# Kernel optimization log

Hardware: AMD Instinct MI355X
Metric: run time of the kernel (lower is better)

Reference implementation:

```python
import jax, jax.numpy as jnp
import numpy as np

C = 512
NH = 8
HD = C // NH
GROUPS = 8
EPS = 1e-5

def group_norm(x, w, b):
    # x: [B,C,H,W], 8 groups
    B, Cc, H, W = x.shape
    xg = x.reshape(B, GROUPS, Cc // GROUPS, H, W)
    mu = xg.mean(axis=(2, 3, 4), keepdims=True)
    var = xg.var(axis=(2, 3, 4), keepdims=True)
    xn = (xg - mu) * jax.lax.rsqrt(var + EPS)
    xn = xn.reshape(B, Cc, H, W)
    return xn * w[None, :, None, None] + b[None, :, None, None]

def conv1x1(x, w, b):
    # w: [O,C], b: [O]
    return jnp.einsum('oc,bchw->bohw', w, x) + b[None, :, None, None]

def setup_inputs() -> dict:
    key = jax.random.key(0)
    ks = jax.random.split(key, 12)
    s = 1.0 / np.sqrt(C)
    inp = {
        'x': jax.random.normal(ks[0], (8, C, 32, 32), dtype=jnp.float32),
        'norm_w': jnp.ones((C,), jnp.float32),
        'norm_b': jnp.zeros((C,), jnp.float32),
        'qw': jax.random.uniform(ks[1], (C, C), jnp.float32, -s, s),
        'qb': jax.random.uniform(ks[2], (C,), jnp.float32, -s, s),
        'kw': jax.random.uniform(ks[3], (C, C), jnp.float32, -s, s),
        'kb': jax.random.uniform(ks[4], (C,), jnp.float32, -s, s),
        'vw': jax.random.uniform(ks[5], (C, C), jnp.float32, -s, s),
        'vb': jax.random.uniform(ks[6], (C,), jnp.float32, -s, s),
        'pw': jax.random.uniform(ks[7], (C, C), jnp.float32, -s, s),
        'pb': jax.random.uniform(ks[8], (C,), jnp.float32, -s, s),
    }
    return inp

def reference(x, norm_w, norm_b, qw, qb, kw, kb, vw, vb, pw, pb):
    b, c, h, w = x.shape
    scale = HD ** (-0.5)
    xn = group_norm(x, norm_w, norm_b)
    q = conv1x1(xn, qw, qb).reshape(b, NH, HD, h * w)
    k = conv1x1(xn, kw, kb).reshape(b, NH, HD, h * w)
    v = conv1x1(xn, vw, vb).reshape(b, NH, HD, h * w)
    attn = jnp.einsum('bhcn,bhcm->bhnm', q, k) * scale
    attn = jax.nn.softmax(attn, axis=-1)
    out = jnp.einsum('bhnm,bhcm->bhcn', attn, v)
    out = out.reshape(b, c, h, w)
    out = conv1x1(out, pw, pb)
    return out + x
```

## Files before the change

kernel.cpp:

```cpp
#include <hip/hip_runtime.h>

#define C_DIM 512
#define N_PIX 1024
#define B_DIM 8
#define NHEAD 8
#define HDIM 64
#define NGRP 8
#define CG 64
#define EPSF 1e-5f

typedef __bf16 bf16x8_t __attribute__((ext_vector_type(8)));
typedef __bf16 bf16x4_t __attribute__((ext_vector_type(4)));
typedef float  f32x4_t  __attribute__((ext_vector_type(4)));
typedef unsigned int u32x4_t __attribute__((ext_vector_type(4)));

__device__ __forceinline__ __bf16 f2b(float f) {
  unsigned int u = __builtin_bit_cast(unsigned int, f);
  u += 0x7fffu + ((u >> 16) & 1u);
  unsigned short s = (unsigned short)(u >> 16);
  return __builtin_bit_cast(__bf16, s);
}

__device__ __forceinline__ unsigned int pack_trunc(float a, float b) {
  return (__builtin_bit_cast(unsigned int, a) >> 16) |
         (__builtin_bit_cast(unsigned int, b) & 0xffff0000u);
}

__device__ __forceinline__ void async16(const void* g, void* l) {
  __builtin_amdgcn_global_load_lds((const __attribute__((address_space(1))) void*)g,
                                   (__attribute__((address_space(3))) void*)l, 16, 0, 0);
}

__global__ __launch_bounds__(256) void prep_kernel(
    const float* __restrict__ qw, const float* __restrict__ kw,
    const float* __restrict__ vw, const float* __restrict__ pw,
    __bf16* __restrict__ wb,
    const float* __restrict__ x, float2* __restrict__ psum)
{
  if (blockIdx.x < 1024) {
    int idx = blockIdx.x * 256 + threadIdx.x;
    int mat = idx >> 16;
    int off = (idx & 65535) * 4;
    const float* src = (mat == 0) ? qw : (mat == 1) ? kw : (mat == 2) ? vw : pw;
    float4 v = *(const float4*)(src + off);
    bf16x4_t pk;
    pk[0] = f2b(v.x); pk[1] = f2b(v.y); pk[2] = f2b(v.z); pk[3] = f2b(v.w);
    *(bf16x4_t*)(wb + mat * (512 * 512) + off) = pk;
  } else {
    const int t = blockIdx.x - 1024;
    const int s = t & 7, bg = t >> 3;
    const float* xp = x + ((size_t)bg * CG + s * 8) * N_PIX;
    float sum = 0.f, sum2 = 0.f;
#pragma unroll
    for (int it = 0; it < 8; it++) {
      float4 v = ((const float4*)xp)[it * 256 + threadIdx.x];
      sum  += v.x + v.y + v.z + v.w;
      sum2 += v.x * v.x + v.y * v.y + v.z * v.z + v.w * v.w;
    }
#pragma unroll
    for (int off = 32; off; off >>= 1) {
      sum  += __shfl_xor(sum, off, 64);
      sum2 += __shfl_xor(sum2, off, 64);
    }
    __shared__ float red[8];
    const int lane = threadIdx.x & 63, wv = threadIdx.x >> 6;
    if (lane == 0) { red[wv] = sum; red[4 + wv] = sum2; }
    __syncthreads();
    if (threadIdx.x == 0) {
      float s1 = red[0] + red[1] + red[2] + red[3];
      float s2 = red[4] + red[5] + red[6] + red[7];
      psum[bg * 8 + s] = make_float2(s1, s2);
    }
  }
}

__global__ __launch_bounds__(256) void gn_apply_kernel(
    const float* __restrict__ x, const float2* __restrict__ psum,
    const float* __restrict__ gw, const float* __restrict__ gb,
    __bf16* __restrict__ xnT)
{
  const int n0 = blockIdx.x * 32, b = blockIdx.y;
  const int tid = threadIdx.x;
  __shared__ float mu_s[8], rs_s[8];
  __shared__ __align__(16) __bf16 tile[32 * 520];

  if (tid < 8) {
    float s1 = 0.f, s2 = 0.f;
#pragma unroll
    for (int i = 0; i < 8; i++) {
      float2 p = psum[(b * 8 + tid) * 8 + i];
      s1 += p.x; s2 += p.y;
    }
    const float inv = 1.f / (float)(CG * N_PIX);
    float mu = s1 * inv;
    float var = s2 * inv - mu * mu;
    mu_s[tid] = mu;
    rs_s[tid] = rsqrtf(var + EPSF);
  }
  __syncthreads();

  const float* xb = x + (size_t)b * C_DIM * N_PIX + n0;
  const int cl = tid >> 3;
  const int nq = (tid & 7) * 4;
#pragma unroll
  for (int co = 0; co < 16; co++) {
    const int c = co * 32 + cl;
    float4 v = *(const float4*)(xb + (size_t)c * N_PIX + nq);
    const int g = c >> 6;
    const float rs = rs_s[g];
    const float a = rs * gw[c];
    const float bb = gb[c] - mu_s[g] * a;
    tile[(nq + 0) * 520 + c] = f2b(v.x * a + bb);
    tile[(nq + 1) * 520 + c] = f2b(v.y * a + bb);
    tile[(nq + 2) * 520 + c] = f2b(v.z * a + bb);
    tile[(nq + 3) * 520 + c] = f2b(v.w * a + bb);
  }
  __syncthreads();

  __bf16* dst = xnT + ((size_t)b * N_PIX + n0) * C_DIM;
  const int l32 = tid & 31, nr = tid >> 5;
#pragma unroll
  for (int no = 0; no < 4; no++) {
    const int n = no * 8 + nr;
#pragma unroll
    for (int co = 0; co < 2; co++) {
      const int c = co * 256 + l32 * 8;
      *(bf16x8_t*)(dst + (size_t)n * C_DIM + c) =
          *(const bf16x8_t*)(tile + n * 520 + c);
    }
  }
}

__device__ __forceinline__ void gemm_core_128(
    const __bf16* __restrict__ A, const __bf16* __restrict__ B,
    __bf16* As, __bf16* Bs, f32x4_t acc[4][4])
{
  const int tid  = threadIdx.x;
  const int lane = tid & 63;
  const int wv   = tid >> 6;
  const int quad = lane >> 4;
  const int l16  = lane & 15;
  const int wm = (wv >> 1) * 64;
  const int wn = (wv & 1) * 64;

  f32x4_t zero = {0.f, 0.f, 0.f, 0.f};
#pragma unroll
  for (int i = 0; i < 4; i++)
#pragma unroll
    for (int j = 0; j < 4; j++) acc[i][j] = zero;

  const int chb0 = wv * 64;
  const int chb1 = 256 + wv * 64;
  const int ch0 = chb0 + lane, ch1 = chb1 + lane;
  const int r0 = ch0 >> 2, k0 = (ch0 & 3) * 8;
  const int r1 = ch1 >> 2, k1 = (ch1 & 3) * 8;

  for (int kt = 0; kt < 512; kt += 32) {
    async16(A + (size_t)r0 * 512 + kt + k0, As + chb0 * 8);
    async16(A + (size_t)r1 * 512 + kt + k1, As + chb1 * 8);
    async16(B + (size_t)r0 * 512 + kt + k0, Bs + chb0 * 8);
    async16(B + (size_t)r1 * 512 + kt + k1, Bs + chb1 * 8);
    __builtin_amdgcn_s_waitcnt(0);
    __syncthreads();
    bf16x8_t af[4], bfr[4];
#pragma unroll
    for (int i = 0; i < 4; i++)
      af[i] = *(const bf16x8_t*)(As + (wm + i * 16 + l16) * 32 + quad * 8);
#pragma unroll
    for (int j = 0; j < 4; j++)
      bfr[j] = *(const bf16x8_t*)(Bs + (wn + j * 16 + l16) * 32 + quad * 8);
#pragma unroll
    for (int i = 0; i < 4; i++)
#pragma unroll
      for (int j = 0; j < 4; j++)
        acc[i][j] = __builtin_amdgcn_mfma_f32_16x16x32_bf16(af[i], bfr[j], acc[i][j], 0, 0, 0);
    __syncthreads();
  }
}

__global__ __launch_bounds__(256) void gemm_qkv_kernel(
    const __bf16* __restrict__ wqkv, const float* __restrict__ qb,
    const float* __restrict__ kb, const float* __restrict__ vb,
    const __bf16* __restrict__ xnT,
    __bf16* __restrict__ qT, __bf16* __restrict__ kT, __bf16* __restrict__ vbuf)
{
  __shared__ __align__(16) __bf16 smem[64 * 132];
  __bf16* As = smem;
  __bf16* Bs = smem + 4096;
  const int b = blockIdx.x;
  const int n0 = blockIdx.y * 128;
  const int mat = blockIdx.z >> 2;
  const int m0 = (blockIdx.z & 3) * 128;
  const __bf16* A = wqkv + (size_t)mat * (512 * 512) + (size_t)m0 * 512;
  const __bf16* B = xnT + ((size_t)b * N_PIX + n0) * 512;
  f32x4_t acc[4][4];
  gemm_core_128(A, B, As, Bs, acc);

  const int tid = threadIdx.x, lane = tid & 63, wv = tid >> 6;
  const int quad = lane >> 4, l16 = lane & 15;
  const int wm = (wv >> 1) * 64, wn = (wv & 1) * 64;
  const float* bias = (mat == 0) ? qb : (mat == 1) ? kb : vb;
  const float qscale = (mat == 0) ? 0.125f * 1.44269504f : 1.0f;

  if (mat < 2) {
    __bf16* dst = (mat == 0) ? qT : kT;
#pragma unroll
    for (int i = 0; i < 4; i++) {
      const int o = m0 + wm + i * 16 + quad * 4;
      float b0 = bias[o], b1 = bias[o + 1], b2 = bias[o + 2], b3 = bias[o + 3];
#pragma unroll
      for (int j = 0; j < 4; j++) {
        const int n = n0 + wn + j * 16 + l16;
        bf16x4_t pk;
        pk[0] = f2b((acc[i][j][0] + b0) * qscale);
        pk[1] = f2b((acc[i][j][1] + b1) * qscale);
        pk[2] = f2b((acc[i][j][2] + b2) * qscale);
        pk[3] = f2b((acc[i][j][3] + b3) * qscale);
        *(bf16x4_t*)(dst + ((size_t)b * N_PIX + n) * 512 + o) = pk;
      }
    }
  } else {
#pragma unroll
    for (int p = 0; p < 2; p++) {
      __syncthreads();
      if ((wv >> 1) == p) {
#pragma unroll
        for (int i = 0; i < 4; i++) {
          const int crow = i * 16 + quad * 4;
          const int o = m0 + p * 64 + crow;
          float b0 = bias[o], b1 = bias[o + 1], b2 = bias[o + 2], b3 = bias[o + 3];
#pragma unroll
          for (int j = 0; j < 4; j++) {
            const int nl = wn + j * 16 + l16;
            smem[(crow + 0) * 132 + nl] = f2b(acc[i][j][0] + b0);
            smem[(crow + 1) * 132 + nl] = f2b(acc[i][j][1] + b1);
            smem[(crow + 2) * 132 + nl] = f2b(acc[i][j][2] + b2);
            smem[(crow + 3) * 132 + nl] = f2b(acc[i][j][3] + b3);
          }
        }
      }
      __syncthreads();
      const int c = tid >> 2;
      const int cg = m0 + p * 64 + c;
      const int nch = (tid & 3) * 32;
      __bf16* vd = vbuf + ((size_t)b * 512 + cg) * N_PIX + n0 + nch;
#pragma unroll
      for (int k = 0; k < 4; k++)
        *(bf16x8_t*)(vd + k * 8) = *(const bf16x8_t*)(smem + c * 132 + nch + k * 8);
    }
  }
}

__global__ __launch_bounds__(256, 4) void attn_kernel(
    const __bf16* __restrict__ qT, const __bf16* __restrict__ kT,
    const __bf16* __restrict__ vbuf, __bf16* __restrict__ aT)
{
  __shared__ __align__(16) __bf16 Ks[64 * 72];
  __shared__ __align__(16) __bf16 Vs[64 * 68];
  const int bh = blockIdx.x;
  const int b = bh >> 3, h = bh & 7;
  const int nb = blockIdx.y;
  const int tid = threadIdx.x, lane = tid & 63, wv = tid >> 6;
  const int quad = lane >> 4, l16 = lane & 15;
  const int n0 = nb * 64;

  const __bf16* qp = qT + ((size_t)b * N_PIX + n0 + wv * 16 + l16) * 512 + h * 64;
  const bf16x8_t qf0 = *(const bf16x8_t*)(qp + quad * 8);
  const bf16x8_t qf1 = *(const bf16x8_t*)(qp + 32 + quad * 8);

  const __bf16* kp = kT + ((size_t)b * N_PIX) * 512 + h * 64;
  const __bf16* vp = vbuf + ((size_t)b * 512 + h * 64) * N_PIX;

  const int srow = tid >> 2, schk = (tid & 3) * 16;
  bf16x8_t kreg0 = *(const bf16x8_t*)(kp + (size_t)srow * 512 + schk);
  bf16x8_t kreg1 = *(const bf16x8_t*)(kp + (size_t)srow * 512 + schk + 8);
  bf16x8_t vreg0 = *(const bf16x8_t*)(vp + (size_t)srow * N_PIX + schk);
  bf16x8_t vreg1 = *(const bf16x8_t*)(vp + (size_t)srow * N_PIX + schk + 8);

  const f32x4_t zero = {0.f, 0.f, 0.f, 0.f};
  f32x4_t oacc[4];
#pragma unroll
  for (int jc = 0; jc < 4; jc++) oacc[jc] = zero;
  f32x4_t lsum4 = zero;

  for (int mt = 0; mt < 16; mt++) {
    __syncthreads();
    *(bf16x8_t*)(Ks + srow * 72 + schk)     = kreg0;
    *(bf16x8_t*)(Ks + srow * 72 + schk + 8) = kreg1;
    *(bf16x8_t*)(Vs + srow * 68 + schk)     = vreg0;
    *(bf16x8_t*)(Vs + srow * 68 + schk + 8) = vreg1;
    __syncthreads();
    if (mt < 15) {
      kreg0 = *(const bf16x8_t*)(kp + (size_t)((mt + 1) * 64 + srow) * 512 + schk);
      kreg1 = *(const bf16x8_t*)(kp + (size_t)((mt + 1) * 64 + srow) * 512 + schk + 8);
      vreg0 = *(const bf16x8_t*)(vp + (size_t)srow * N_PIX + (mt + 1) * 64 + schk);
      vreg1 = *(const bf16x8_t*)(vp + (size_t)srow * N_PIX + (mt + 1) * 64 + schk + 8);
    }

    f32x4_t sacc[4];
#pragma unroll
    for (int mb = 0; mb < 4; mb++) {
      sacc[mb] = zero;
      bf16x8_t kf0 = *(const bf16x8_t*)(Ks + (mb * 16 + l16) * 72 + quad * 8);
      bf16x8_t kf1 = *(const bf16x8_t*)(Ks + (mb * 16 + l16) * 72 + 32 + quad * 8);
      sacc[mb] = __builtin_amdgcn_mfma_f32_16x16x32_bf16(kf0, qf0, sacc[mb], 0, 0, 0);
      sacc[mb] = __builtin_amdgcn_mfma_f32_16x16x32_bf16(kf1, qf1, sacc[mb], 0, 0, 0);
    }

    float p[4][4];
#pragma unroll
    for (int mb = 0; mb < 4; mb++)
#pragma unroll
      for (int r = 0; r < 4; r++) {
        p[mb][r] = __builtin_amdgcn_exp2f(sacc[mb][r]);
        lsum4[r] += p[mb][r];
      }

    bf16x8_t pf[2];
#pragma unroll
    for (int pr = 0; pr < 2; pr++) {
      u32x4_t u;
      u[0] = pack_trunc(p[2 * pr][0],     p[2 * pr][1]);
      u[1] = pack_trunc(p[2 * pr][2],     p[2 * pr][3]);
      u[2] = pack_trunc(p[2 * pr + 1][0], p[2 * pr + 1][1]);
      u[3] = pack_trunc(p[2 * pr + 1][2], p[2 * pr + 1][3]);
      pf[pr] = __builtin_bit_cast(bf16x8_t, u);
    }

#pragma unroll
    for (int jc = 0; jc < 4; jc++) {
      const int vrow = (jc * 16 + l16) * 68;
#pragma unroll
      for (int pr = 0; pr < 2; pr++) {
        bf16x4_t vlo = *(const bf16x4_t*)(Vs + vrow + pr * 32 + quad * 4);
        bf16x4_t vhi = *(const bf16x4_t*)(Vs + vrow + pr * 32 + 16 + quad * 4);
        bf16x8_t vf;
#pragma unroll
        for (int r = 0; r < 4; r++) { vf[r] = vlo[r]; vf[4 + r] = vhi[r]; }
        oacc[jc] = __builtin_amdgcn_mfma_f32_16x16x32_bf16(vf, pf[pr], oacc[jc], 0, 0, 0);
      }
    }
  }

  float lsum = lsum4[0] + lsum4[1] + lsum4[2] + lsum4[3];
  lsum += __shfl_xor(lsum, 16, 64);
  lsum += __shfl_xor(lsum, 32, 64);
  const float inv = 1.f / lsum;

  __bf16* op = aT + ((size_t)b * N_PIX + n0 + wv * 16 + l16) * 512 + h * 64;
#pragma unroll
  for (int jc = 0; jc < 4; jc++) {
    bf16x4_t o4;
#pragma unroll
    for (int r = 0; r < 4; r++) o4[r] = f2b(oacc[jc][r] * inv);
    *(bf16x4_t*)(op + jc * 16 + quad * 4) = o4;
  }
}

__global__ __launch_bounds__(256) void gemm_proj_kernel(
    const __bf16* __restrict__ wp, const float* __restrict__ pb,
    const __bf16* __restrict__ aT, const float* __restrict__ x,
    float* __restrict__ out)
{
  __shared__ __align__(16) __bf16 As[128 * 32];
  __shared__ __align__(16) __bf16 Bs[128 * 32];
  const int b = blockIdx.x;
  const int n0 = blockIdx.y * 128;
  const int m0 = blockIdx.z * 128;
  const __bf16* A = wp + (size_t)m0 * 512;
  const __bf16* B = aT + ((size_t)b * N_PIX + n0) * 512;
  f32x4_t acc[4][4];
  gemm_core_128(A, B, As, Bs, acc);
  const int tid = threadIdx.x, lane = tid & 63, wv = tid >> 6;
  const int quad = lane >> 4, l16 = lane & 15;
  const int wm = (wv >> 1) * 64, wn = (wv & 1) * 64;
#pragma unroll
  for (int i = 0; i < 4; i++) {
    const int o = m0 + wm + i * 16 + quad * 4;
#pragma unroll
    for (int j = 0; j < 4; j++) {
      const int n = n0 + wn + j * 16 + l16;
#pragma unroll
      for (int r = 0; r < 4; r++) {
        size_t idx = ((size_t)b * 512 + o + r) * N_PIX + n;
        out[idx] = acc[i][j][r] + pb[o + r] + x[idx];
      }
    }
  }
}

extern "C" void kernel_launch(void* const* d_in, const int* in_sizes, int n_in,
                              void* d_out, int out_size, void* d_ws, size_t ws_size,
                              hipStream_t stream)
{
  (void)in_sizes; (void)n_in; (void)out_size; (void)ws_size;
  const float* x   = (const float*)d_in[0];
  const float* gnw = (const float*)d_in[1];
  const float* gnb = (const float*)d_in[2];
  const float* qw  = (const float*)d_in[3];
  const float* qb  = (const float*)d_in[4];
  const float* kw  = (const float*)d_in[5];
  const float* kb  = (const float*)d_in[6];
  const float* vw  = (const float*)d_in[7];
  const float* vb  = (const float*)d_in[8];
  const float* pw  = (const float*)d_in[9];
  const float* pb  = (const float*)d_in[10];
  float* out = (float*)d_out;

  char* ws = (char*)d_ws;
  __bf16* wb   = (__bf16*)(ws);
  __bf16* xnT  = (__bf16*)(ws + (size_t)(2  << 20));
  __bf16* qTb  = (__bf16*)(ws + (size_t)(10 << 20));
  __bf16* kTb  = (__bf16*)(ws + (size_t)(18 << 20));
  __bf16* vbf  = (__bf16*)(ws + (size_t)(26 << 20));
  __bf16* aT   = (__bf16*)(ws + (size_t)(34 << 20));
  float2* psum = (float2*)(ws + (size_t)(42 << 20));

  hipLaunchKernelGGL(prep_kernel, dim3(1536), dim3(256), 0, stream,
                     qw, kw, vw, pw, wb, x, psum);
  hipLaunchKernelGGL(gn_apply_kernel, dim3(32, 8), dim3(256), 0, stream, x, psum, gnw, gnb, xnT);
  hipLaunchKernelGGL(gemm_qkv_kernel, dim3(8, 8, 12), dim3(256), 0, stream,
                     wb, qb, kb, vb, xnT, qTb, kTb, vbf);
  hipLaunchKernelGGL(attn_kernel, dim3(64, 16), dim3(256), 0, stream, qTb, kTb, vbf, aT);
  hipLaunchKernelGGL(gemm_proj_kernel, dim3(8, 8, 4), dim3(256), 0, stream,
                     wb + (size_t)3 * 512 * 512, pb, aT, x, out);
}
```

Baseline: 168.6 us.

## Double GEMM k-step, widen attention query tile, pre-permute V in shared memory

The shared GEMM core now loads two 32-wide k-slices per barrier pair (k-step 64), which halves the number of synchronisations, and the shared-memory buffers grow to match. The attention kernel handles 128 queries per block (32 per wave), so each K/V tile staged in LDS is reused across twice as many queries and the grid is halved. V is stored in LDS in a permuted layout so each MFMA operand comes from a single 16-byte read instead of two 8-byte reads plus a shuffle. In exchange, register pressure goes up (launch bounds drop to 2 blocks per CU) and there are fewer blocks to fill the device.

Result: no change. 169.9 us (+0.8%).

```diff
diff --git a/kernel.cpp b/kernel.cpp
--- a/kernel.cpp
+++ b/kernel.cpp
@@ -149,31 +149,37 @@
 #pragma unroll
     for (int j = 0; j < 4; j++) acc[i][j] = zero;
 
-  const int chb0 = wv * 64;
-  const int chb1 = 256 + wv * 64;
+  const int chb0 = wv * 128;
+  const int chb1 = wv * 128 + 64;
   const int ch0 = chb0 + lane, ch1 = chb1 + lane;
   const int r0 = ch0 >> 2, k0 = (ch0 & 3) * 8;
   const int r1 = ch1 >> 2, k1 = (ch1 & 3) * 8;
 
-  for (int kt = 0; kt < 512; kt += 32) {
-    async16(A + (size_t)r0 * 512 + kt + k0, As + chb0 * 8);
-    async16(A + (size_t)r1 * 512 + kt + k1, As + chb1 * 8);
-    async16(B + (size_t)r0 * 512 + kt + k0, Bs + chb0 * 8);
-    async16(B + (size_t)r1 * 512 + kt + k1, Bs + chb1 * 8);
+  for (int kt = 0; kt < 512; kt += 64) {
+#pragma unroll
+    for (int p = 0; p < 2; p++) {
+      async16(A + (size_t)r0 * 512 + kt + p * 32 + k0, As + p * 4096 + chb0 * 8);
+      async16(A + (size_t)r1 * 512 + kt + p * 32 + k1, As + p * 4096 + chb1 * 8);
+      async16(B + (size_t)r0 * 512 + kt + p * 32 + k0, Bs + p * 4096 + chb0 * 8);
+      async16(B + (size_t)r1 * 512 + kt + p * 32 + k1, Bs + p * 4096 + chb1 * 8);
+    }
     __builtin_amdgcn_s_waitcnt(0);
     __syncthreads();
-    bf16x8_t af[4], bfr[4];
-#pragma unroll
-    for (int i = 0; i < 4; i++)
-      af[i] = *(const bf16x8_t*)(As + (wm + i * 16 + l16) * 32 + quad * 8);
-#pragma unroll
-    for (int j = 0; j < 4; j++)
-      bfr[j] = *(const bf16x8_t*)(Bs + (wn + j * 16 + l16) * 32 + quad * 8);
-#pragma unroll
-    for (int i = 0; i < 4; i++)
+#pragma unroll
+    for (int p = 0; p < 2; p++) {
+      bf16x8_t af[4], bfr[4];
+#pragma unroll
+      for (int i = 0; i < 4; i++)
+        af[i] = *(const bf16x8_t*)(As + p * 4096 + (wm + i * 16 + l16) * 32 + quad * 8);
 #pragma unroll
       for (int j = 0; j < 4; j++)
-        acc[i][j] = __builtin_amdgcn_mfma_f32_16x16x32_bf16(af[i], bfr[j], acc[i][j], 0, 0, 0);
+        bfr[j] = *(const bf16x8_t*)(Bs + p * 4096 + (wn + j * 16 + l16) * 32 + quad * 8);
+#pragma unroll
+      for (int i = 0; i < 4; i++)
+#pragma unroll
+        for (int j = 0; j < 4; j++)
+          acc[i][j] = __builtin_amdgcn_mfma_f32_16x16x32_bf16(af[i], bfr[j], acc[i][j], 0, 0, 0);
+    }
     __syncthreads();
   }
 }
@@ -184,9 +190,9 @@
     const __bf16* __restrict__ xnT,
     __bf16* __restrict__ qT, __bf16* __restrict__ kT, __bf16* __restrict__ vbuf)
 {
-  __shared__ __align__(16) __bf16 smem[64 * 132];
+  __shared__ __align__(16) __bf16 smem[16384];
   __bf16* As = smem;
-  __bf16* Bs = smem + 4096;
+  __bf16* Bs = smem + 8192;
   const int b = blockIdx.x;
   const int n0 = blockIdx.y * 128;
   const int mat = blockIdx.z >> 2;
@@ -251,109 +257,135 @@
   }
 }
 
-__global__ __launch_bounds__(256, 4) void attn_kernel(
+__global__ __launch_bounds__(256, 2) void attn_kernel(
     const __bf16* __restrict__ qT, const __bf16* __restrict__ kT,
     const __bf16* __restrict__ vbuf, __bf16* __restrict__ aT)
 {
   __shared__ __align__(16) __bf16 Ks[64 * 72];
-  __shared__ __align__(16) __bf16 Vs[64 * 68];
+  __shared__ __align__(16) __bf16 Vp[64 * 72];
   const int bh = blockIdx.x;
-  const int b = bh >> 3, h = bh & 7;
-  const int nb = blockIdx.y;
+  const int b = bh >> 3, head = bh & 7;
+  const int n0 = blockIdx.y * 128;
   const int tid = threadIdx.x, lane = tid & 63, wv = tid >> 6;
   const int quad = lane >> 4, l16 = lane & 15;
-  const int n0 = nb * 64;
-
-  const __bf16* qp = qT + ((size_t)b * N_PIX + n0 + wv * 16 + l16) * 512 + h * 64;
-  const bf16x8_t qf0 = *(const bf16x8_t*)(qp + quad * 8);
-  const bf16x8_t qf1 = *(const bf16x8_t*)(qp + 32 + quad * 8);
-
-  const __bf16* kp = kT + ((size_t)b * N_PIX) * 512 + h * 64;
-  const __bf16* vp = vbuf + ((size_t)b * 512 + h * 64) * N_PIX;
-
-  const int srow = tid >> 2, schk = (tid & 3) * 16;
-  bf16x8_t kreg0 = *(const bf16x8_t*)(kp + (size_t)srow * 512 + schk);
-  bf16x8_t kreg1 = *(const bf16x8_t*)(kp + (size_t)srow * 512 + schk + 8);
-  bf16x8_t vreg0 = *(const bf16x8_t*)(vp + (size_t)srow * N_PIX + schk);
-  bf16x8_t vreg1 = *(const bf16x8_t*)(vp + (size_t)srow * N_PIX + schk + 8);
+
+  bf16x8_t qf[2][2];
+#pragma unroll
+  for (int qt = 0; qt < 2; qt++) {
+    const __bf16* qp = qT + ((size_t)b * N_PIX + n0 + wv * 32 + qt * 16 + l16) * 512 + head * 64;
+    qf[qt][0] = *(const bf16x8_t*)(qp + quad * 8);
+    qf[qt][1] = *(const bf16x8_t*)(qp + 32 + quad * 8);
+  }
+
+  const __bf16* kp = kT + ((size_t)b * N_PIX) * 512 + head * 64;
+  const __bf16* vp = vbuf + ((size_t)b * 512 + head * 64) * N_PIX;
+
+  const int srow = tid >> 2, scol = (tid & 3) * 16;
+  const int pr0 = scol >> 5, hh0 = (scol >> 4) & 1;
+  const int pos0 = pr0 * 32 + (((scol >> 2) & 3) | 0) * 8 + hh0 * 4;
+  const int mc1 = scol + 8;
+  const int pr1 = mc1 >> 5, hh1 = (mc1 >> 4) & 1;
+  const int pos1 = pr1 * 32 + ((mc1 >> 2) & 3) * 8 + hh1 * 4;
+
+  bf16x8_t kreg0 = *(const bf16x8_t*)(kp + (size_t)srow * 512 + scol);
+  bf16x8_t kreg1 = *(const bf16x8_t*)(kp + (size_t)srow * 512 + scol + 8);
+  bf16x8_t vreg0 = *(const bf16x8_t*)(vp + (size_t)srow * N_PIX + scol);
+  bf16x8_t vreg1 = *(const bf16x8_t*)(vp + (size_t)srow * N_PIX + scol + 8);
 
   const f32x4_t zero = {0.f, 0.f, 0.f, 0.f};
-  f32x4_t oacc[4];
-#pragma unroll
-  for (int jc = 0; jc < 4; jc++) oacc[jc] = zero;
-  f32x4_t lsum4 = zero;
+  f32x4_t oacc[2][4];
+#pragma unroll
+  for (int qt = 0; qt < 2; qt++)
+#pragma unroll
+    for (int jc = 0; jc < 4; jc++) oacc[qt][jc] = zero;
+  f32x4_t lsum4[2] = {zero, zero};
 
   for (int mt = 0; mt < 16; mt++) {
     __syncthreads();
-    *(bf16x8_t*)(Ks + srow * 72 + schk)     = kreg0;
-    *(bf16x8_t*)(Ks + srow * 72 + schk + 8) = kreg1;
-    *(bf16x8_t*)(Vs + srow * 68 + schk)     = vreg0;
-    *(bf16x8_t*)(Vs + srow * 68 + schk + 8) = vreg1;
+    *(bf16x8_t*)(Ks + srow * 72 + scol)     = kreg0;
+    *(bf16x8_t*)(Ks + srow * 72 + scol + 8) = kreg1;
+    {
+      bf16x4_t lo, hi;
+#pragma unroll
+      for (int r = 0; r < 4; r++) { lo[r] = vreg0[r]; hi[r] = vreg0[4 + r]; }
+      *(bf16x4_t*)(Vp + srow * 72 + pos0)     = lo;
+      *(bf16x4_t*)(Vp + srow * 72 + pos0 + 8) = hi;
+#pragma unroll
+      for (int r = 0; r < 4; r++) { lo[r] = vreg1[r]; hi[r] = vreg1[4 + r]; }
+      *(bf16x4_t*)(Vp + srow * 72 + pos1)     = lo;
+      *(bf16x4_t*)(Vp + srow * 72 + pos1 + 8) = hi;
+    }
     __syncthreads();
     if (mt < 15) {
-      kreg0 = *(const bf16x8_t*)(kp + (size_t)((mt + 1) * 64 + srow) * 512 + schk);
-      kreg1 = *(const bf16x8_t*)(kp + (size_t)((mt + 1) * 64 + srow) * 512 + schk + 8);
-      vreg0 = *(const bf16x8_t*)(vp + (size_t)srow * N_PIX + (mt + 1) * 64 + schk);
-      vreg1 = *(const bf16x8_t*)(vp + (size_t)srow * N_PIX + (mt + 1) * 64 + schk + 8);
-    }
-
-    f32x4_t sacc[4];
+      kreg0 = *(const bf16x8_t*)(kp + (size_t)((mt + 1) * 64 + srow) * 512 + scol);
+      kreg1 = *(const bf16x8_t*)(kp + (size_t)((mt + 1) * 64 + srow) * 512 + scol + 8);
+      vreg0 = *(const bf16x8_t*)(vp + (size_t)srow * N_PIX + (mt + 1) * 64 + scol);
+      vreg1 = *(const bf16x8_t*)(vp + (size_t)srow * N_PIX + (mt + 1) * 64 + scol + 8);
+    }
+
+    f32x4_t sacc[2][4];
 #pragma unroll
     for (int mb = 0; mb < 4; mb++) {
-      sacc[mb] = zero;
       bf16x8_t kf0 = *(const bf16x8_t*)(Ks + (mb * 16 + l16) * 72 + quad * 8);
       bf16x8_t kf1 = *(const bf16x8_t*)(Ks + (mb * 16 + l16) * 72 + 32 + quad * 8);
-      sacc[mb] = __builtin_amdgcn_mfma_f32_16x16x32_bf16(kf0, qf0, sacc[mb], 0, 0, 0);
-      sacc[mb] = __builtin_amdgcn_mfma_f32_16x16x32_bf16(kf1, qf1, sacc[mb], 0, 0, 0);
-    }
-
-    float p[4][4];
-#pragma unroll
-    for (int mb = 0; mb < 4; mb++)
-#pragma unroll
-      for (int r = 0; r < 4; r++) {
-        p[mb][r] = __builtin_amdgcn_exp2f(sacc[mb][r]);
-        lsum4[r] += p[mb][r];
-      }
-
-    bf16x8_t pf[2];
-#pragma unroll
-    for (int pr = 0; pr < 2; pr++) {
-      u32x4_t u;
-      u[0] = pack_trunc(p[2 * pr][0],     p[2 * pr][1]);
-      u[1] = pack_trunc(p[2 * pr][2],     p[2 * pr][3]);
-      u[2] = pack_trunc(p[2 * pr + 1][0], p[2 * pr + 1][1]);
-      u[3] = pack_trunc(p[2 * pr + 1][2], p[2 * pr + 1][3]);
-      pf[pr] = __builtin_bit_cast(bf16x8_t, u);
+#pragma unroll
+      for (int qt = 0; qt < 2; qt++) {
+        f32x4_t s = zero;
+        s = __builtin_amdgcn_mfma_f32_16x16x32_bf16(kf0, qf[qt][0], s, 0, 0, 0);
+        s = __builtin_amdgcn_mfma_f32_16x16x32_bf16(kf1, qf[qt][1], s, 0, 0, 0);
+        sacc[qt][mb] = s;
+      }
+    }
+
+    bf16x8_t pf[2][2];
+#pragma unroll
+    for (int qt = 0; qt < 2; qt++) {
+      float p[4][4];
+#pragma unroll
+      for (int mb = 0; mb < 4; mb++)
+#pragma unroll
+        for (int r = 0; r < 4; r++) {
+          p[mb][r] = __builtin_amdgcn_exp2f(sacc[qt][mb][r]);
+          lsum4[qt][r] += p[mb][r];
+        }
+#pragma unroll
+      for (int pr = 0; pr < 2; pr++) {
+        u32x4_t u;
+        u[0] = pack_trunc(p[2 * pr][0],     p[2 * pr][1]);
+        u[1] = pack_trunc(p[2 * pr][2],     p[2 * pr][3]);
+        u[2] = pack_trunc(p[2 * pr + 1][0], p[2 * pr + 1][1]);
+        u[3] = pack_trunc(p[2 * pr + 1][2], p[2 * pr + 1][3]);
+        pf[qt][pr] = __builtin_bit_cast(bf16x8_t, u);
+      }
     }
 
 #pragma unroll
     for (int jc = 0; jc < 4; jc++) {
-      const int vrow = (jc * 16 + l16) * 68;
+      const int vrow = (jc * 16 + l16) * 72;
 #pragma unroll
       for (int pr = 0; pr < 2; pr++) {
-        bf16x4_t vlo = *(const bf16x4_t*)(Vs + vrow + pr * 32 + quad * 4);
-        bf16x4_t vhi = *(const bf16x4_t*)(Vs + vrow + pr * 32 + 16 + quad * 4);
-        bf16x8_t vf;
-#pragma unroll
-        for (int r = 0; r < 4; r++) { vf[r] = vlo[r]; vf[4 + r] = vhi[r]; }
-        oacc[jc] = __builtin_amdgcn_mfma_f32_16x16x32_bf16(vf, pf[pr], oacc[jc], 0, 0, 0);
-      }
-    }
-  }
-
-  float lsum = lsum4[0] + lsum4[1] + lsum4[2] + lsum4[3];
-  lsum += __shfl_xor(lsum, 16, 64);
-  lsum += __shfl_xor(lsum, 32, 64);
-  const float inv = 1.f / lsum;
-
-  __bf16* op = aT + ((size_t)b * N_PIX + n0 + wv * 16 + l16) * 512 + h * 64;
-#pragma unroll
-  for (int jc = 0; jc < 4; jc++) {
-    bf16x4_t o4;
-#pragma unroll
-    for (int r = 0; r < 4; r++) o4[r] = f2b(oacc[jc][r] * inv);
-    *(bf16x4_t*)(op + jc * 16 + quad * 4) = o4;
+        bf16x8_t vf = *(const bf16x8_t*)(Vp + vrow + pr * 32 + quad * 8);
+#pragma unroll
+        for (int qt = 0; qt < 2; qt++)
+          oacc[qt][jc] = __builtin_amdgcn_mfma_f32_16x16x32_bf16(vf, pf[qt][pr], oacc[qt][jc], 0, 0, 0);
+      }
+    }
+  }
+
+#pragma unroll
+  for (int qt = 0; qt < 2; qt++) {
+    float lsum = lsum4[qt][0] + lsum4[qt][1] + lsum4[qt][2] + lsum4[qt][3];
+    lsum += __shfl_xor(lsum, 16, 64);
+    lsum += __shfl_xor(lsum, 32, 64);
+    const float inv = 1.f / lsum;
+    __bf16* op = aT + ((size_t)b * N_PIX + n0 + wv * 32 + qt * 16 + l16) * 512 + head * 64;
+#pragma unroll
+    for (int jc = 0; jc < 4; jc++) {
+      bf16x4_t o4;
+#pragma unroll
+      for (int r = 0; r < 4; r++) o4[r] = f2b(oacc[qt][jc][r] * inv);
+      *(bf16x4_t*)(op + jc * 16 + quad * 4) = o4;
+    }
   }
 }
 
@@ -362,8 +394,8 @@
     const __bf16* __restrict__ aT, const float* __restrict__ x,
     float* __restrict__ out)
 {
-  __shared__ __align__(16) __bf16 As[128 * 32];
-  __shared__ __align__(16) __bf16 Bs[128 * 32];
+  __shared__ __align__(16) __bf16 As[8192];
+  __shared__ __align__(16) __bf16 Bs[8192];
   const int b = blockIdx.x;
   const int n0 = blockIdx.y * 128;
   const int m0 = blockIdx.z * 128;
@@ -421,7 +453,7 @@
   hipLaunchKernelGGL(gn_apply_kernel, dim3(32, 8), dim3(256), 0, stream, x, psum, gnw, gnb, xnT);
   hipLaunchKernelGGL(gemm_qkv_kernel, dim3(8, 8, 12), dim3(256), 0, stream,
                      wb, qb, kb, vb, xnT, qTb, kTb, vbf);
-  hipLaunchKernelGGL(attn_kernel, dim3(64, 16), dim3(256), 0, stream, qTb, kTb, vbf, aT);
+  hipLaunchKernelGGL(attn_kernel, dim3(64, 8), dim3(256), 0, stream, qTb, kTb, vbf, aT);
   hipLaunchKernelGGL(gemm_proj_kernel, dim3(8, 8, 4), dim3(256), 0, stream,
                      wb + (size_t)3 * 512 * 512, pb, aT, x, out);
 }
```
